# Kernel tuning notes

Hardware: AMD Instinct MI355X
Metric: run time of the kernel (lower is better)

Reference implementation:

```python
import jax, jax.numpy as jnp
import numpy as np
from jax import lax


def ternary_quantize(w):
    # alpha = mean(|w|); threshold = 0.7*alpha; map to {-1,0,1}*alpha
    alpha = jnp.mean(jnp.abs(w))
    threshold = 0.7 * alpha
    w_ternary = jnp.where(jnp.abs(w) < threshold, jnp.zeros_like(w), jnp.sign(w))
    return alpha * w_ternary


def setup_inputs() -> dict:
    key = jax.random.key(0)
    k1, k2 = jax.random.split(key)
    B, L, Cin = 32, 8192, 1
    K, F = 16, 256
    x = jax.random.normal(k1, (B, L, Cin), dtype=jnp.float32)
    # matches keras RandomUniform(-0.1, 0.1) initializer
    w = jax.random.uniform(k2, (K, Cin, F), dtype=jnp.float32, minval=-0.1, maxval=0.1)
    b = jnp.zeros((F,), dtype=jnp.float32)
    return {"x": x, "w": w, "b": b}


def reference(x, w, b):
    # x: (B, L, Cin) NWC; w: (K, Cin, F) WIO; stride 1, padding SAME
    w_q = ternary_quantize(w)
    y = lax.conv_general_dilated(
        x, w_q,
        window_strides=(1,),
        padding="SAME",
        dimension_numbers=("NWC", "WIO", "NWC"),
    )
    return y + b
```

## Files before the change

kernel.cpp:

```cpp
#include <hip/hip_runtime.h>
#include <hip/hip_bf16.h>

__global__ __launch_bounds__(256) void ternary_quant_kernel(
    const float* __restrict__ w, float* __restrict__ wq, int n) {
    __shared__ float red[256];
    __shared__ float alpha_s;
    const int tid = threadIdx.x;
    float s = 0.f;
    for (int i = tid; i < n; i += 256) s += fabsf(w[i]);
    red[tid] = s;
    __syncthreads();
    for (int off = 128; off > 0; off >>= 1) {
        if (tid < off) red[tid] += red[tid + off];
        __syncthreads();
    }
    if (tid == 0) alpha_s = red[0] / (float)n;
    __syncthreads();
    const float alpha = alpha_s;
    const float thr = 0.7f * alpha;
    for (int i = tid; i < n; i += 256) {
        float v = w[i];
        float t = (fabsf(v) < thr) ? 0.f : (v > 0.f ? 1.f : (v < 0.f ? -1.f : 0.f));
        wq[i] = alpha * t;
    }
}

__global__ __launch_bounds__(256) void ternary_conv1d_kernel(
    const float* __restrict__ x,
    const float* __restrict__ wq,
    const float* __restrict__ bias,
    float* __restrict__ y,
    int L, int ltiles) {
    const int f = threadIdx.x;
    const int bid = blockIdx.x;
    const int lt = bid % ltiles;
    const int b  = bid / ltiles;
    const int l0 = lt * 64;

    __shared__ float xs[80];
    if (f < 79) {
        int gl = l0 - 7 + f;
        xs[f] = (gl >= 0 && gl < L) ? x[(size_t)b * L + gl] : 0.f;
    }

    float wqr[16];
#pragma unroll
    for (int k = 0; k < 16; ++k) wqr[k] = wq[k * 256 + f];
    const float bf = bias[f];

    __syncthreads();

    float* out = y + ((size_t)b * L + l0) * 256 + f;
#pragma unroll
    for (int c = 0; c < 4; ++c) {
        float xv[31];
#pragma unroll
        for (int i = 0; i < 31; ++i) xv[i] = xs[c * 16 + i];
#pragma unroll
        for (int l = 0; l < 16; ++l) {
            float acc = bf;
#pragma unroll
            for (int k = 0; k < 16; ++k) acc = fmaf(wqr[k], xv[l + k], acc);
            out[(size_t)(c * 16 + l) * 256] = acc;
        }
    }
}

extern "C" void kernel_launch(void* const* d_in, const int* in_sizes, int n_in,
                              void* d_out, int out_size, void* d_ws, size_t ws_size,
                              hipStream_t stream) {
    const float* x = (const float*)d_in[0];
    const float* w = (const float*)d_in[1];
    const float* b = (const float*)d_in[2];
    float* y = (float*)d_out;
    float* wq = (float*)d_ws;

    const int B = 32;
    const int L = in_sizes[0] / B;
    const int nW = in_sizes[1];
    const int ltiles = L / 64;

    ternary_quant_kernel<<<1, 256, 0, stream>>>(w, wq, nW);
    ternary_conv1d_kernel<<<B * ltiles, 256, 0, stream>>>(x, wq, b, y, L, ltiles);
}
```

Before: 57.09 us.

## Vectorize conv output to float4 nontemporal stores with 4 filters per thread

Each thread of the conv kernel now computes 4 adjacent filters and 16 positions, interleaved as positions ls, ls+4, ..., using float4 weight loads and float4 nontemporal stores. A sliding register window over the shared input is shifted by 4 at each step. The goal is fewer, wider global stores on an output-write-bound kernel, with nontemporal hints so the streaming output does not pollute the cache. The quantization kernel is also widened from 256 to 1024 threads.

```diff
diff --git a/kernel.cpp b/kernel.cpp
--- a/kernel.cpp
+++ b/kernel.cpp
@@ -1,16 +1,18 @@
 #include <hip/hip_runtime.h>
 #include <hip/hip_bf16.h>
 
-__global__ __launch_bounds__(256) void ternary_quant_kernel(
+typedef float f32x4 __attribute__((ext_vector_type(4)));
+
+__global__ __launch_bounds__(1024) void ternary_quant_kernel(
     const float* __restrict__ w, float* __restrict__ wq, int n) {
-    __shared__ float red[256];
+    __shared__ float red[1024];
     __shared__ float alpha_s;
     const int tid = threadIdx.x;
     float s = 0.f;
-    for (int i = tid; i < n; i += 256) s += fabsf(w[i]);
+    for (int i = tid; i < n; i += 1024) s += fabsf(w[i]);
     red[tid] = s;
     __syncthreads();
-    for (int off = 128; off > 0; off >>= 1) {
+    for (int off = 512; off > 0; off >>= 1) {
         if (tid < off) red[tid] += red[tid + off];
         __syncthreads();
     }
@@ -18,7 +20,7 @@
     __syncthreads();
     const float alpha = alpha_s;
     const float thr = 0.7f * alpha;
-    for (int i = tid; i < n; i += 256) {
+    for (int i = tid; i < n; i += 1024) {
         float v = w[i];
         float t = (fabsf(v) < thr) ? 0.f : (v > 0.f ? 1.f : (v < 0.f ? -1.f : 0.f));
         wq[i] = alpha * t;
@@ -31,37 +33,47 @@
     const float* __restrict__ bias,
     float* __restrict__ y,
     int L, int ltiles) {
-    const int f = threadIdx.x;
+    const int t  = threadIdx.x;
+    const int fg = t & 63;
+    const int ls = t >> 6;
     const int bid = blockIdx.x;
     const int lt = bid % ltiles;
     const int b  = bid / ltiles;
     const int l0 = lt * 64;
 
     __shared__ float xs[80];
-    if (f < 79) {
-        int gl = l0 - 7 + f;
-        xs[f] = (gl >= 0 && gl < L) ? x[(size_t)b * L + gl] : 0.f;
+    if (t < 79) {
+        int gl = l0 - 7 + t;
+        xs[t] = (gl >= 0 && gl < L) ? x[(size_t)b * L + gl] : 0.f;
     }
 
-    float wqr[16];
+    f32x4 wv[16];
 #pragma unroll
-    for (int k = 0; k < 16; ++k) wqr[k] = wq[k * 256 + f];
-    const float bf = bias[f];
+    for (int k = 0; k < 16; ++k)
+        wv[k] = *reinterpret_cast<const f32x4*>(wq + k * 256 + fg * 4);
+    const f32x4 bv = *reinterpret_cast<const f32x4*>(bias + fg * 4);
 
     __syncthreads();
 
-    float* out = y + ((size_t)b * L + l0) * 256 + f;
+    float xw[16];
 #pragma unroll
-    for (int c = 0; c < 4; ++c) {
-        float xv[31];
+    for (int j = 0; j < 16; ++j) xw[j] = xs[ls + j];
+
+    f32x4* outp = reinterpret_cast<f32x4*>(y) + ((size_t)b * L + l0 + ls) * 64 + fg;
 #pragma unroll
-        for (int i = 0; i < 31; ++i) xv[i] = xs[c * 16 + i];
+    for (int i = 0; i < 16; ++i) {
+        f32x4 acc = bv;
 #pragma unroll
-        for (int l = 0; l < 16; ++l) {
-            float acc = bf;
+        for (int k = 0; k < 16; ++k) {
+            acc += wv[k] * xw[k];
+        }
+        __builtin_nontemporal_store(acc, outp);
+        outp += 256;
+        if (i < 15) {
 #pragma unroll
-            for (int k = 0; k < 16; ++k) acc = fmaf(wqr[k], xv[l + k], acc);
-            out[(size_t)(c * 16 + l) * 256] = acc;
+            for (int j = 0; j < 12; ++j) xw[j] = xw[j + 4];
+#pragma unroll
+            for (int j = 12; j < 16; ++j) xw[j] = xs[ls + 4 * (i + 1) + j];
         }
     }
 }
@@ -80,6 +92,6 @@
     const int nW = in_sizes[1];
     const int ltiles = L / 64;
 
-    ternary_quant_kernel<<<1, 256, 0, stream>>>(w, wq, nW);
+    ternary_quant_kernel<<<1, 1024, 0, stream>>>(w, wq, nW);
     ternary_conv1d_kernel<<<B * ltiles, 256, 0, stream>>>(x, wq, b, y, L, ltiles);
 }
```

New measurement: 65.98 us. 15.6% more time.
